# Kernel optimization log

Measured on AMD Instinct MI355X. Metric: run time of the kernel, lower is better.

The kernel has to match this reference:

```python
import jax, jax.numpy as jnp
import numpy as np

TEMPERATURE = 1.0        # sample_codebook_temperature
COMMITMENT_COST = 1.0

B, T, D, K = 8, 4096, 64, 1024


def setup_inputs() -> dict:
    key = jax.random.key(0)
    k1, k2 = jax.random.split(key)
    x = jax.random.normal(k1, (B, T, D), dtype=jnp.float32)
    embeddings = jax.random.normal(k2, (D, K), dtype=jnp.float32)  # (embedding_dim, codebook_size)
    return {"x": x, "embeddings": embeddings}


def gumbel_softmax(logits, temperature):
    # logits: [N, K]
    K_ = logits.shape[1]
    indices = jnp.argmax(logits, axis=1)
    enc = jax.nn.one_hot(indices, K_, dtype=logits.dtype)
    pi0 = jax.nn.softmax(logits, axis=-1)
    pi1 = (enc + jax.nn.softmax(logits / temperature, axis=-1)) / 2
    pi1 = jax.nn.softmax(jax.lax.stop_gradient(jnp.log(pi1) - logits), axis=1)
    pi2 = 2 * pi1 - 0.5 * pi0
    encodings = pi2 - jax.lax.stop_gradient(pi2) + enc  # straight-through encodings
    return indices, encodings


def reference(x, embeddings):
    D_, K_ = embeddings.shape
    flat = x.reshape(-1, D_)                              # [N, D]
    # squared euclidean distances via matmul (cdist trick)
    sim = flat @ embeddings                               # [N, K]
    dist = (jnp.sum(flat ** 2, axis=1, keepdims=True)
            - 2.0 * sim
            + jnp.sum(embeddings ** 2, axis=0, keepdims=True))
    indices, encodings = gumbel_softmax(-dist, TEMPERATURE)
    indices = indices.reshape(x.shape[:-1])               # [B, T]
    quantized = embeddings.T[indices]                     # gather: [B, T, D]
    e_latent_loss = jnp.mean(jnp.square(jax.lax.stop_gradient(quantized) - x))
    loss = e_latent_loss * COMMITMENT_COST
    # straight-through estimator (training-mode output; same values as eval)
    quantized = x + jax.lax.stop_gradient(quantized - x)
    return quantized, encodings, indices, loss
```

## Files before the change

kernel.cpp:

```cpp
#include <hip/hip_runtime.h>
#include <hip/hip_bf16.h>


#define NROWS 32768
#define DDIM 64
#define KCB 1024

#define WS_ET    0
#define WS_H     65536
#define WS_LACC  66560
#define WS_PBEST 66564
#define WS_PIDX  197636
#define WS_IBEST 328708

__global__ __launch_bounds__(256) void k1_prep(const float* __restrict__ E,
                                               float* __restrict__ Et,
                                               float* __restrict__ h,
                                               float* __restrict__ lacc) {
  int k = blockIdx.x * 256 + threadIdx.x;
  float col[DDIM];
  float sum = 0.f;
#pragma unroll
  for (int d = 0; d < DDIM; ++d) {
    float v = E[d * KCB + k];
    col[d] = v;
    sum = fmaf(v, v, sum);
  }
  float4* dst = (float4*)(Et + (size_t)k * DDIM);
#pragma unroll
  for (int i = 0; i < 16; ++i)
    dst[i] = make_float4(col[4*i], col[4*i+1], col[4*i+2], col[4*i+3]);
  h[k] = 0.5f * sum;
  if (k == 0) lacc[0] = 0.f;
}

__global__ __launch_bounds__(256) void k2_score(const float* __restrict__ x,
                                                const float* __restrict__ Et,
                                                const float* __restrict__ h,
                                                float* __restrict__ pbest,
                                                int* __restrict__ pidx) {
  int bid = blockIdx.x;
  int kq  = bid & 3;
  int n   = (bid >> 2) * 256 + threadIdx.x;

  const float4* xr = (const float4*)(x + (size_t)n * DDIM);
  float4 xv[16];
#pragma unroll
  for (int i = 0; i < 16; ++i) xv[i] = xr[i];

  const float4* Ef4 = (const float4*)Et;
  int kbase = kq * 256;
  float best = -3.0e38f;
  int besti = kbase;

  for (int k0 = kbase; k0 < kbase + 256; k0 += 8) {
    float acc[8];
#pragma unroll
    for (int j = 0; j < 8; ++j) acc[j] = -h[k0 + j];
#pragma unroll
    for (int i = 0; i < 16; ++i) {
      float4 xi = xv[i];
#pragma unroll
      for (int j = 0; j < 8; ++j) {
        float4 e4 = Ef4[(k0 + j) * 16 + i];
        acc[j] = fmaf(xi.x, e4.x, acc[j]);
        acc[j] = fmaf(xi.y, e4.y, acc[j]);
        acc[j] = fmaf(xi.z, e4.z, acc[j]);
        acc[j] = fmaf(xi.w, e4.w, acc[j]);
      }
    }
#pragma unroll
    for (int j = 0; j < 8; ++j) {
      if (acc[j] > best) { best = acc[j]; besti = k0 + j; }
    }
  }
  pbest[kq * NROWS + n] = best;
  pidx [kq * NROWS + n] = besti;
}

__global__ __launch_bounds__(256) void k3_finalize(const float* __restrict__ x,
                                                   const float* __restrict__ Et,
                                                   const float* __restrict__ pbest,
                                                   const int* __restrict__ pidx,
                                                   float* __restrict__ lacc,
                                                   int* __restrict__ ibest,
                                                   float* __restrict__ out_q,
                                                   float* __restrict__ out_ind) {
  int n = blockIdx.x * 256 + threadIdx.x;
  float best = pbest[n];
  int bi = pidx[n];
#pragma unroll
  for (int q = 1; q < 4; ++q) {
    float b = pbest[q * NROWS + n];
    int i2 = pidx[q * NROWS + n];
    if (b > best) { best = b; bi = i2; }
  }
  ibest[n] = bi;
  out_ind[n] = (float)bi;

  const float4* xr = (const float4*)(x + (size_t)n * DDIM);
  const float4* qr = (const float4*)(Et + (size_t)bi * DDIM);
  float lsum = 0.f;
#pragma unroll
  for (int i = 0; i < 16; ++i) {
    float4 q4 = qr[i];
    float4 x4 = xr[i];
    float d0 = q4.x - x4.x, d1 = q4.y - x4.y, d2 = q4.z - x4.z, d3 = q4.w - x4.w;
    lsum = fmaf(d0, d0, lsum); lsum = fmaf(d1, d1, lsum);
    lsum = fmaf(d2, d2, lsum); lsum = fmaf(d3, d3, lsum);
    *(float4*)(out_q + (size_t)n * DDIM + i * 4) = q4;
  }

#pragma unroll
  for (int off = 32; off > 0; off >>= 1) lsum += __shfl_down(lsum, off);
  __shared__ float red[4];
  int lane = threadIdx.x & 63, w = threadIdx.x >> 6;
  if (lane == 0) red[w] = lsum;
  __syncthreads();
  if (threadIdx.x == 0) atomicAdd(lacc, red[0] + red[1] + red[2] + red[3]);
}

__global__ __launch_bounds__(256) void k4_enc(const int* __restrict__ ibest,
                                              float* __restrict__ out_enc) {
  int t = threadIdx.x;
  int r0 = blockIdx.x * 16;
#pragma unroll
  for (int r = 0; r < 16; ++r) {
    int row = r0 + r;
    int bk = ibest[row];
    bool hit = (bk >> 2) == t;
    int j = bk & 3;
    float4 v;
    v.x = (hit && j == 0) ? 1.0f : 0.0f;
    v.y = (hit && j == 1) ? 1.0f : 0.0f;
    v.z = (hit && j == 2) ? 1.0f : 0.0f;
    v.w = (hit && j == 3) ? 1.0f : 0.0f;
    *(float4*)(out_enc + (size_t)row * KCB + t * 4) = v;
  }
}

__global__ void k5_loss(const float* __restrict__ lacc, float* __restrict__ out_loss) {
  out_loss[0] = lacc[0] * (1.0f / 2097152.0f);
}

extern "C" void kernel_launch(void* const* d_in, const int* in_sizes, int n_in,
                              void* d_out, int out_size, void* d_ws, size_t ws_size,
                              hipStream_t stream) {
  const float* x = (const float*)d_in[0];
  const float* E = (const float*)d_in[1];

  float* ws    = (float*)d_ws;
  float* Et    = ws + WS_ET;
  float* h     = ws + WS_H;
  float* lacc  = ws + WS_LACC;
  float* pbest = ws + WS_PBEST;
  int*   pidx  = (int*)(ws + WS_PIDX);
  int*   ibest = (int*)(ws + WS_IBEST);

  float* out      = (float*)d_out;
  float* out_q    = out;
  float* out_enc  = out + 2097152;
  float* out_ind  = out + 35651584;
  float* out_loss = out + 35684352;

  k1_prep<<<4, 256, 0, stream>>>(E, Et, h, lacc);
  k2_score<<<512, 256, 0, stream>>>(x, Et, h, pbest, pidx);
  k3_finalize<<<128, 256, 0, stream>>>(x, Et, pbest, pidx, lacc, ibest, out_q, out_ind);
  k4_enc<<<2048, 256, 0, stream>>>(ibest, out_enc);
  k5_loss<<<1, 1, 0, stream>>>(lacc, out_loss);
}
```

Before: 262.2 us.

## Fuse finalize, one-hot encoding and loss into one kernel; split codebook into 8 segments

The codebook scan now runs over 8 segments of 128 codes instead of 4 of 256, giving 1024 scoring blocks with a launch-bounds occupancy hint. Partial indices are stored as 16-bit values. The finalize, one-hot write and loss kernels are merged into one kernel: 16 threads per block reduce and gather, then all threads write one-hot rows with nontemporal stores. The last block, found via an atomic counter, writes the loss, which removes two launches but leaves only 16 active threads in the gather phase.

```diff
diff --git a/kernel.cpp b/kernel.cpp
--- a/kernel.cpp
+++ b/kernel.cpp
@@ -3,20 +3,25 @@
 
 
 #define NROWS 32768
-#define DDIM 64
-#define KCB 1024
+#define DDIM  64
+#define KCB   1024
+#define NSEG  8
+#define SEG   128
+
+typedef float f32x4 __attribute__((ext_vector_type(4)));
 
 #define WS_ET    0
 #define WS_H     65536
 #define WS_LACC  66560
+#define WS_CTR   66561
 #define WS_PBEST 66564
-#define WS_PIDX  197636
-#define WS_IBEST 328708
+#define WS_PIDX  328708
 
 __global__ __launch_bounds__(256) void k1_prep(const float* __restrict__ E,
                                                float* __restrict__ Et,
                                                float* __restrict__ h,
-                                               float* __restrict__ lacc) {
+                                               float* __restrict__ lacc,
+                                               unsigned int* __restrict__ ctr) {
   int k = blockIdx.x * 256 + threadIdx.x;
   float col[DDIM];
   float sum = 0.f;
@@ -31,17 +36,17 @@
   for (int i = 0; i < 16; ++i)
     dst[i] = make_float4(col[4*i], col[4*i+1], col[4*i+2], col[4*i+3]);
   h[k] = 0.5f * sum;
-  if (k == 0) lacc[0] = 0.f;
+  if (k == 0) { lacc[0] = 0.f; ctr[0] = 0u; }
 }
 
-__global__ __launch_bounds__(256) void k2_score(const float* __restrict__ x,
-                                                const float* __restrict__ Et,
-                                                const float* __restrict__ h,
-                                                float* __restrict__ pbest,
-                                                int* __restrict__ pidx) {
+__global__ __launch_bounds__(256, 4) void k2_score(const float* __restrict__ x,
+                                                   const float* __restrict__ Et,
+                                                   const float* __restrict__ h,
+                                                   float* __restrict__ pbest,
+                                                   unsigned short* __restrict__ pidx) {
   int bid = blockIdx.x;
-  int kq  = bid & 3;
-  int n   = (bid >> 2) * 256 + threadIdx.x;
+  int ks  = bid >> 7;
+  int n   = (bid & 127) * 256 + threadIdx.x;
 
   const float4* xr = (const float4*)(x + (size_t)n * DDIM);
   float4 xv[16];
@@ -49,11 +54,11 @@
   for (int i = 0; i < 16; ++i) xv[i] = xr[i];
 
   const float4* Ef4 = (const float4*)Et;
-  int kbase = kq * 256;
+  int kbase = ks * SEG;
   float best = -3.0e38f;
   int besti = kbase;
 
-  for (int k0 = kbase; k0 < kbase + 256; k0 += 8) {
+  for (int k0 = kbase; k0 < kbase + SEG; k0 += 8) {
     float acc[8];
 #pragma unroll
     for (int j = 0; j < 8; ++j) acc[j] = -h[k0 + j];
@@ -74,73 +79,75 @@
       if (acc[j] > best) { best = acc[j]; besti = k0 + j; }
     }
   }
-  pbest[kq * NROWS + n] = best;
-  pidx [kq * NROWS + n] = besti;
+  pbest[ks * NROWS + n] = best;
+  pidx [ks * NROWS + n] = (unsigned short)besti;
 }
 
-__global__ __launch_bounds__(256) void k3_finalize(const float* __restrict__ x,
-                                                   const float* __restrict__ Et,
-                                                   const float* __restrict__ pbest,
-                                                   const int* __restrict__ pidx,
-                                                   float* __restrict__ lacc,
-                                                   int* __restrict__ ibest,
-                                                   float* __restrict__ out_q,
-                                                   float* __restrict__ out_ind) {
-  int n = blockIdx.x * 256 + threadIdx.x;
-  float best = pbest[n];
-  int bi = pidx[n];
+__global__ __launch_bounds__(256) void k3_fused(const float* __restrict__ x,
+                                                const float* __restrict__ Et,
+                                                const float* __restrict__ pbest,
+                                                const unsigned short* __restrict__ pidx,
+                                                float* __restrict__ lacc,
+                                                unsigned int* __restrict__ ctr,
+                                                float* __restrict__ out_q,
+                                                float* __restrict__ out_enc,
+                                                float* __restrict__ out_ind,
+                                                float* __restrict__ out_loss) {
+  __shared__ int sidx[16];
+  int tid = threadIdx.x;
+  int r0 = blockIdx.x * 16;
+
+  float lsum = 0.f;
+  if (tid < 16) {
+    int n = r0 + tid;
+    float best = pbest[n];
+    int bi = pidx[n];
 #pragma unroll
-  for (int q = 1; q < 4; ++q) {
-    float b = pbest[q * NROWS + n];
-    int i2 = pidx[q * NROWS + n];
-    if (b > best) { best = b; bi = i2; }
+    for (int q = 1; q < NSEG; ++q) {
+      float b = pbest[q * NROWS + n];
+      int i2 = (int)pidx[q * NROWS + n];
+      if (b > best) { best = b; bi = i2; }
+    }
+    sidx[tid] = bi;
+    out_ind[n] = (float)bi;
+
+    const float4* xr = (const float4*)(x + (size_t)n * DDIM);
+    const float4* qr = (const float4*)(Et + (size_t)bi * DDIM);
+    float4* qw = (float4*)(out_q + (size_t)n * DDIM);
+#pragma unroll
+    for (int i = 0; i < 16; ++i) {
+      float4 q4 = qr[i];
+      float4 x4 = xr[i];
+      float d0 = q4.x - x4.x, d1 = q4.y - x4.y, d2 = q4.z - x4.z, d3 = q4.w - x4.w;
+      lsum = fmaf(d0, d0, lsum); lsum = fmaf(d1, d1, lsum);
+      lsum = fmaf(d2, d2, lsum); lsum = fmaf(d3, d3, lsum);
+      qw[i] = q4;
+    }
   }
-  ibest[n] = bi;
-  out_ind[n] = (float)bi;
+#pragma unroll
+  for (int off = 8; off > 0; off >>= 1) lsum += __shfl_down(lsum, off);
+  if (tid == 0) atomicAdd(lacc, lsum);
+  __syncthreads();
 
-  const float4* xr = (const float4*)(x + (size_t)n * DDIM);
-  const float4* qr = (const float4*)(Et + (size_t)bi * DDIM);
-  float lsum = 0.f;
 #pragma unroll
-  for (int i = 0; i < 16; ++i) {
-    float4 q4 = qr[i];
-    float4 x4 = xr[i];
-    float d0 = q4.x - x4.x, d1 = q4.y - x4.y, d2 = q4.z - x4.z, d3 = q4.w - x4.w;
-    lsum = fmaf(d0, d0, lsum); lsum = fmaf(d1, d1, lsum);
-    lsum = fmaf(d2, d2, lsum); lsum = fmaf(d3, d3, lsum);
-    *(float4*)(out_q + (size_t)n * DDIM + i * 4) = q4;
+  for (int r = 0; r < 16; ++r) {
+    int bk = sidx[r];
+    f32x4 v = (f32x4)(0.f);
+    if ((bk >> 2) == tid) {
+      int j = bk & 3;
+      v[j] = 1.0f;
+    }
+    __builtin_nontemporal_store(v, (f32x4*)(out_enc + (size_t)(r0 + r) * KCB + tid * 4));
   }
 
-#pragma unroll
-  for (int off = 32; off > 0; off >>= 1) lsum += __shfl_down(lsum, off);
-  __shared__ float red[4];
-  int lane = threadIdx.x & 63, w = threadIdx.x >> 6;
-  if (lane == 0) red[w] = lsum;
-  __syncthreads();
-  if (threadIdx.x == 0) atomicAdd(lacc, red[0] + red[1] + red[2] + red[3]);
-}
-
-__global__ __launch_bounds__(256) void k4_enc(const int* __restrict__ ibest,
-                                              float* __restrict__ out_enc) {
-  int t = threadIdx.x;
-  int r0 = blockIdx.x * 16;
-#pragma unroll
-  for (int r = 0; r < 16; ++r) {
-    int row = r0 + r;
-    int bk = ibest[row];
-    bool hit = (bk >> 2) == t;
-    int j = bk & 3;
-    float4 v;
-    v.x = (hit && j == 0) ? 1.0f : 0.0f;
-    v.y = (hit && j == 1) ? 1.0f : 0.0f;
-    v.z = (hit && j == 2) ? 1.0f : 0.0f;
-    v.w = (hit && j == 3) ? 1.0f : 0.0f;
-    *(float4*)(out_enc + (size_t)row * KCB + t * 4) = v;
+  if (tid == 0) {
+    __threadfence();
+    unsigned int old = atomicAdd(ctr, 1u);
+    if (old == (unsigned int)(gridDim.x - 1)) {
+      float total = atomicAdd(lacc, 0.0f);
+      out_loss[0] = total * (1.0f / 2097152.0f);
+    }
   }
-}
-
-__global__ void k5_loss(const float* __restrict__ lacc, float* __restrict__ out_loss) {
-  out_loss[0] = lacc[0] * (1.0f / 2097152.0f);
 }
 
 extern "C" void kernel_launch(void* const* d_in, const int* in_sizes, int n_in,
@@ -153,9 +160,9 @@
   float* Et    = ws + WS_ET;
   float* h     = ws + WS_H;
   float* lacc  = ws + WS_LACC;
+  unsigned int* ctr = (unsigned int*)(ws + WS_CTR);
   float* pbest = ws + WS_PBEST;
-  int*   pidx  = (int*)(ws + WS_PIDX);
-  int*   ibest = (int*)(ws + WS_IBEST);
+  unsigned short* pidx = (unsigned short*)(ws + WS_PIDX);
 
   float* out      = (float*)d_out;
   float* out_q    = out;
@@ -163,9 +170,8 @@
   float* out_ind  = out + 35651584;
   float* out_loss = out + 35684352;
 
-  k1_prep<<<4, 256, 0, stream>>>(E, Et, h, lacc);
-  k2_score<<<512, 256, 0, stream>>>(x, Et, h, pbest, pidx);
-  k3_finalize<<<128, 256, 0, stream>>>(x, Et, pbest, pidx, lacc, ibest, out_q, out_ind);
-  k4_enc<<<2048, 256, 0, stream>>>(ibest, out_enc);
-  k5_loss<<<1, 1, 0, stream>>>(lacc, out_loss);
+  k1_prep<<<4, 256, 0, stream>>>(E, Et, h, lacc, ctr);
+  k2_score<<<1024, 256, 0, stream>>>(x, Et, h, pbest, pidx);
+  k3_fused<<<2048, 256, 0, stream>>>(x, Et, pbest, pidx, lacc, ctr,
+                                     out_q, out_enc, out_ind, out_loss);
 }
```

Result: slower. 335.3 us (+27.8%).
